# Kernel optimization log

Hardware: AMD Instinct MI355X
Metric: run time of the kernel (lower is better)

## Reference

```python
import jax, jax.numpy as jnp
import numpy as np

NX = 320   # image matrix (nRead)
NC = 8     # coils
NT = 8     # motion states
M = 65536  # non-Cartesian k-space samples per frame
OS = 2     # gridding oversampling factor


def setup_inputs() -> dict:
    key = jax.random.key(0)
    ks = jax.random.split(key, 7)
    kspace_r = jax.random.normal(ks[0], (NC, M), jnp.float32)
    kspace_i = jax.random.normal(ks[1], (NC, M), jnp.float32)
    # k-space trajectory normalized to [-0.5, 0.5)
    traj = jax.random.uniform(ks[2], (M, 2, NT), jnp.float32, -0.5, 0.5)
    csm_r = jax.random.normal(ks[3], (NC, NX, NX), jnp.float32)
    csm_i = jax.random.normal(ks[4], (NC, NX, NX), jnp.float32)
    dcf = jax.random.uniform(ks[5], (M, NT), jnp.float32)
    # motion/flow field in pixels, [NX, NX, 2, NT]
    motions = 3.0 * jax.random.normal(ks[6], (NX, NX, 2, NT), jnp.float32)
    return dict(kspace_r=kspace_r, kspace_i=kspace_i, traj=traj,
                csm_r=csm_r, csm_i=csm_i, dcf=dcf, motions=motions)


def _grid_adjoint(kspace, traj_t, dcf_t, csm):
    """Adjoint NUFFT (gpuNUFFT adj_op): density-compensated bilinear gridding
    onto a 2x oversampled Cartesian grid, inverse FFT, center crop,
    deapodization, and conjugate coil combination."""
    G = OS * NX
    data = (kspace * dcf_t[None, :]).astype(jnp.complex64)  # [NC, M]
    u = (traj_t[:, 0] + 0.5) * G
    v = (traj_t[:, 1] + 0.5) * G
    u0 = jnp.floor(u)
    v0 = jnp.floor(v)
    du = (u - u0).astype(jnp.float32)
    dv = (v - v0).astype(jnp.float32)
    i0 = u0.astype(jnp.int32) % G
    i1 = (i0 + 1) % G
    j0 = v0.astype(jnp.int32) % G
    j1 = (j0 + 1) % G
    grid = jnp.zeros((NC, G, G), jnp.complex64)
    grid = grid.at[:, i0, j0].add(data * ((1.0 - du) * (1.0 - dv)))
    grid = grid.at[:, i1, j0].add(data * (du * (1.0 - dv)))
    grid = grid.at[:, i0, j1].add(data * ((1.0 - du) * dv))
    grid = grid.at[:, i1, j1].add(data * (du * dv))
    im_os = jnp.fft.fftshift(
        jnp.fft.ifft2(jnp.fft.ifftshift(grid, axes=(-2, -1)), axes=(-2, -1)),
        axes=(-2, -1))
    s = (G - NX) // 2
    im = im_os[:, s:s + NX, s:s + NX]  # [NC, NX, NX]
    # deapodization: FT of the triangle (bilinear) gridding kernel is sinc^2
    x = (jnp.arange(NX, dtype=jnp.float32) - NX // 2) / G
    d = jnp.sinc(x) ** 2
    im = im / (d[:, None] * d[None, :])
    # conjugate coil combine with sensitivity maps
    return jnp.sum(jnp.conj(csm) * im, axis=0).astype(jnp.complex64)


def _bilinear_warp(im, flow):
    """apply_sparse_motion: sparse bilinear-interpolation warp of a 2D image
    by a per-pixel displacement field flow[..., 0:2] (in pixels)."""
    Nx, Ny = im.shape
    xs = jnp.arange(Nx, dtype=jnp.float32)[:, None] + flow[..., 0]
    ys = jnp.arange(Ny, dtype=jnp.float32)[None, :] + flow[..., 1]
    xs = jnp.clip(xs, 0.0, Nx - 1.0)
    ys = jnp.clip(ys, 0.0, Ny - 1.0)
    x0 = jnp.floor(xs).astype(jnp.int32)
    y0 = jnp.floor(ys).astype(jnp.int32)
    x1 = jnp.minimum(x0 + 1, Nx - 1)
    y1 = jnp.minimum(y0 + 1, Ny - 1)
    dx = xs - x0.astype(jnp.float32)
    dy = ys - y0.astype(jnp.float32)
    return ((1.0 - dx) * (1.0 - dy) * im[x0, y0]
            + dx * (1.0 - dy) * im[x1, y0]
            + (1.0 - dx) * dy * im[x0, y1]
            + dx * dy * im[x1, y1])


def reference(kspace_r, kspace_i, traj, csm_r, csm_i, dcf, motions):
    kspace = (kspace_r + 1j * kspace_i).astype(jnp.complex64)
    csm = (csm_r + 1j * csm_i).astype(jnp.complex64)

    def frame(traj_t, dcf_t, flow_t):
        im = _grid_adjoint(kspace, traj_t, dcf_t, csm)
        return _bilinear_warp(im, flow_t)

    # vmap over motion states: traj[..., t], dcf[..., t], motions[..., t]
    per_frame = jax.vmap(frame, in_axes=(2, 1, 3))(traj, dcf, motions)  # [NT, NX, NX]
    out = jnp.sum(per_frame, axis=0)  # temporal sum, complex [NX, NX]
    return jnp.stack([out.real, out.imag], axis=-1)  # [NX, NX, 2]
```

## Files before the change

kernel.cpp:

```cpp
#include <hip/hip_runtime.h>
#include <math.h>

#define NXI 320
#define NCI 8
#define NTI 8
#define MI  65536
#define GI  640
#define G2I (GI*GI)
#define NPIX (NXI*NXI)
#define REC_F 20
#define NBINS (NTI*G2I)
#define SCAN_BLKS2 (NBINS/4096)

typedef float v2f __attribute__((ext_vector_type(2)));

__device__ inline v2f cmul(v2f a, v2f b) {
    v2f axx = __builtin_shufflevector(a, a, 0, 0);
    v2f ayy = __builtin_shufflevector(a, a, 1, 1);
    v2f byx = __builtin_shufflevector(b, b, 1, 0);
    v2f r = axx * b;
    v2f t = ayy * byx;
    return r + v2f{-t.x, t.y};
}

template<int H>
__device__ inline float sxf(float x) {
    if constexpr (H == 1) {
        return __int_as_float(__builtin_amdgcn_update_dpp(
            __float_as_int(x), __float_as_int(x), 0xB1, 0xF, 0xF, false));
    } else if constexpr (H == 2) {
        return __int_as_float(__builtin_amdgcn_update_dpp(
            __float_as_int(x), __float_as_int(x), 0x4E, 0xF, 0xF, false));
    } else if constexpr (H == 8) {
        return __int_as_float(__builtin_amdgcn_update_dpp(
            __float_as_int(x), __float_as_int(x), 0x128, 0xF, 0xF, false));
    } else {
        return __shfl_xor(x, H, 64);
    }
}
template<int H>
__device__ inline v2f sxv(v2f v) { return v2f{sxf<H>(v.x), sxf<H>(v.y)}; }

__device__ inline void cell_of(const float* __restrict__ traj, int m, int f,
                               int& i0s, int& j0s, float& du, float& dv)
{
    float tu = traj[(m*2 + 0)*NTI + f];
    float tv = traj[(m*2 + 1)*NTI + f];
    float u = (tu + 0.5f) * (float)GI;
    float v = (tv + 0.5f) * (float)GI;
    float fu = floorf(u), fv = floorf(v);
    du = u - fu; dv = v - fv;
    i0s = (int)fu + GI/2; if (i0s >= GI) i0s -= GI;
    j0s = (int)fv + GI/2; if (j0s >= GI) j0s -= GI;
}

__global__ __launch_bounds__(256) void count_cells(
    const float* __restrict__ traj, int* __restrict__ counts)
{
    int tid = blockIdx.x * 256 + threadIdx.x;
    int f = tid >> 16, m = tid & (MI - 1);
    int i0s, j0s; float du, dv;
    cell_of(traj, m, f, i0s, j0s, du, dv);
    atomicAdd(&counts[f*G2I + i0s*GI + j0s], 1);
}

__device__ inline int wave_incl_scan(int v, int lane) {
    #pragma unroll
    for (int d = 1; d < 64; d <<= 1) {
        int y = __shfl_up(v, d, 64);
        if (lane >= d) v += y;
    }
    return v;
}

__global__ __launch_bounds__(1024) void scanA(const int4* __restrict__ counts4,
                                              int4* __restrict__ binstart4,
                                              int* __restrict__ sums)
{
    __shared__ int wtot[16];
    int tid = threadIdx.x, lane = tid & 63, wv = tid >> 6;
    int i = blockIdx.x * 1024 + tid;
    int4 c = counts4[i];
    int s = c.x + c.y + c.z + c.w;
    int incl = wave_incl_scan(s, lane);
    if (lane == 63) wtot[wv] = incl;
    __syncthreads();
    if (wv == 0 && lane < 16) {
        int t = wtot[lane];
        #pragma unroll
        for (int d = 1; d < 16; d <<= 1) {
            int y = __shfl_up(t, d, 64);
            if (lane >= d) t += y;
        }
        wtot[lane] = t;
    }
    __syncthreads();
    int woff = wv ? wtot[wv - 1] : 0;
    int excl = woff + incl - s;
    int4 b;
    b.x = excl; b.y = excl + c.x; b.z = b.y + c.y; b.w = b.z + c.z;
    binstart4[i] = b;
    if (tid == 1023) sums[blockIdx.x] = woff + incl;
}

__global__ __launch_bounds__(1024) void scanB(int* __restrict__ sums,
                                              int* __restrict__ binstart)
{
    __shared__ int tmp[1024];
    int tid = threadIdx.x;
    int v = (tid < SCAN_BLKS2) ? sums[tid] : 0;
    tmp[tid] = v; __syncthreads();
    for (int d = 1; d < 1024; d <<= 1) {
        int y = (tid >= d) ? tmp[tid - d] : 0;
        __syncthreads();
        tmp[tid] += y;
        __syncthreads();
    }
    int incl = tmp[tid];
    if (tid < SCAN_BLKS2) sums[tid] = incl - v;
    if (tid == SCAN_BLKS2 - 1) {
        sums[SCAN_BLKS2] = incl;
        binstart[NBINS] = 0;
    }
}

__global__ __launch_bounds__(256) void scatter_cells(
    const float* __restrict__ kr, const float* __restrict__ ki,
    const float* __restrict__ traj, const float* __restrict__ dcf,
    int* __restrict__ counts, const int* __restrict__ binstart,
    const int* __restrict__ sums, float* __restrict__ recs)
{
    int tid = blockIdx.x * 256 + threadIdx.x;
    int f = tid >> 16, m = tid & (MI - 1);
    int i0s, j0s; float du, dv;
    cell_of(traj, m, f, i0s, j0s, du, dv);
    float w = dcf[m*NTI + f];
    int bin = f*G2I + i0s*GI + j0s;
    int within = atomicSub(&counts[bin], 1) - 1;
    int slot = binstart[bin] + sums[bin >> 12] + within;
    float4* r = (float4*)(recs + (size_t)slot * REC_F);
    r[0] = make_float4(du, 1.f - du, dv, 1.f - dv);
    #pragma unroll
    for (int q = 0; q < 4; ++q) {
        int c0 = 2*q;
        r[1+q] = make_float4(kr[c0*MI + m]*w,     ki[c0*MI + m]*w,
                             kr[(c0+1)*MI + m]*w, ki[(c0+1)*MI + m]*w);
    }
}

__device__ inline void dft5p(v2f x0, v2f x1, v2f x2, v2f x3, v2f x4, v2f* X)
{
    const float c1 = 0.309016994f, c2 = -0.809016994f;
    const float s1 = 0.951056516f, s2 =  0.587785252f;
    v2f S1 = x1 + x4, D1 = x1 - x4;
    v2f S2 = x2 + x3, D2 = x2 - x3;
    X[0] = x0 + S1 + S2;
    v2f A = x0 + c1*S1 + c2*S2;
    v2f T = s1*D1 + s2*D2;
    v2f B = x0 + c2*S1 + c1*S2;
    v2f U = s2*D1 - s1*D2;
    v2f iT = v2f{-T.y, T.x};
    v2f iU = v2f{-U.y, U.x};
    X[1] = A + iT;  X[4] = A - iT;
    X[2] = B + iU;  X[3] = B - iU;
}

template<int H, int S>
__device__ inline void bf_stage(v2f* a, int lane)
{
    const float PI = 3.14159265358979f;
    bool low = (lane & H) == 0;
    int kp = (lane << S) & 31;
    float sn, cs;
    __sincosf((2.0f * PI / 64.0f) * (float)kp, &sn, &cs);
    v2f w = low ? v2f{1.f, 0.f} : v2f{cs, sn};
    float sg = low ? 1.f : -1.f;
    v2f sgv = v2f{sg, sg};
    #pragma unroll
    for (int n = 0; n < 10; ++n) {
        v2f p = sxv<H>(a[n]);
        v2f t = sgv * a[n] + p;
        a[n] = cmul(t, w);
    }
}

__device__ inline void fft640_pruned(v2f* a, int lane, v2f* line, int xorm)
{
    const float PI = 3.14159265358979f;
    bf_stage<32, 0>(a, lane);
    bf_stage<16, 1>(a, lane);
    bf_stage< 8, 2>(a, lane);
    bf_stage< 4, 3>(a, lane);
    bf_stage< 2, 4>(a, lane);
    bf_stage< 1, 5>(a, lane);
    int k1 = __brev(lane) >> 26;
    float th2 = (2.0f * PI / 640.0f) * (float)k1;
    float sn, cs;
    __sincosf(th2, &sn, &cs);
    v2f wb = v2f{cs, sn};
    v2f w = wb;
    #pragma unroll
    for (int n = 1; n < 10; ++n) {
        a[n] = cmul(a[n], w);
        w = cmul(w, wb);
    }
    v2f E[5], O[5];
    dft5p(a[0], a[2], a[4], a[6], a[8], E);
    dft5p(a[1], a[3], a[5], a[7], a[9], O);
    const v2f tk1 = { 0.809016994f, 0.587785252f};
    const v2f tk2 = { 0.309016994f, 0.951056516f};
    const v2f tk3 = {-0.309016994f, 0.951056516f};
    const v2f tk4 = {-0.809016994f, 0.587785252f};
    v2f t1 = cmul(tk1, O[1]);
    v2f t2 = cmul(tk2, O[2]);
    v2f t3 = cmul(tk3, O[3]);
    v2f t4 = cmul(tk4, O[4]);
    bool hi = (k1 >= 32);
    line[(160 + k1) ^ xorm] = E[0] + O[0];
    line[(224 + k1) ^ xorm] = E[1] + t1;
    int yx = hi ? (k1 - 32) : (288 + k1);
    v2f zx = hi ? (E[2] - t2) : (E[2] + t2);
    line[yx ^ xorm] = zx;
    line[(32 + k1) ^ xorm] = E[3] - t3;
    line[(96 + k1) ^ xorm] = E[4] - t4;
}

__global__ __launch_bounds__(512, 8) void row_fft(
    const int* __restrict__ binstart, const int* __restrict__ sums,
    const float* __restrict__ recs, v2f* __restrict__ rowout)
{
    __shared__ v2f A[NCI][GI];
    int bid = blockIdx.x;
    int i = bid % GI;
    int f = bid / GI;
    int tid = threadIdx.x;
    int im1 = i ? i - 1 : GI - 1;
    const int base0 = f*G2I + i*GI;
    const int base1 = f*G2I + im1*GI;

    #define GS(b) (binstart[b] + sums[(b) >> 12])

    for (int j = tid; j < GI; j += 512) {
        v2f acc[NCI];
        #pragma unroll
        for (int c = 0; c < NCI; ++c) acc[c] = v2f{0.f, 0.f};
        if (j > 0) {
            int lo0 = GS(base0 + j - 1), mid0 = GS(base0 + j), hi0 = GS(base0 + j + 1);
            int lo1 = GS(base1 + j - 1), mid1 = GS(base1 + j), hi1 = GS(base1 + j + 1);
            int L0 = hi0 - lo0;
            int K  = L0 + (hi1 - lo1);
            for (int k = 0; k < K; ++k) {
                bool p1 = (k >= L0);
                int  s   = p1 ? (lo1 + (k - L0)) : (lo0 + k);
                int  mid = p1 ? mid1 : mid0;
                const float4* R = (const float4*)(recs + (size_t)s*REC_F);
                float4 h4 = R[0];
                float wr = p1 ? h4.x : h4.y;
                float w  = wr * ((s < mid) ? h4.z : h4.w);
                float4 d0 = R[1], d1 = R[2], d2 = R[3], d3 = R[4];
                acc[0] += w * v2f{d0.x, d0.y};  acc[1] += w * v2f{d0.z, d0.w};
                acc[2] += w * v2f{d1.x, d1.y};  acc[3] += w * v2f{d1.z, d1.w};
                acc[4] += w * v2f{d2.x, d2.y};  acc[5] += w * v2f{d2.z, d2.w};
                acc[6] += w * v2f{d3.x, d3.y};  acc[7] += w * v2f{d3.z, d3.w};
            }
        } else {
            #pragma unroll
            for (int p = 0; p < 2; ++p) {
                const int base = p ? base1 : base0;
                #pragma unroll
                for (int side = 0; side < 2; ++side) {
                    int b = base + (side ? 0 : (GI - 1));
                    int s0 = GS(b), s1 = GS(b + 1);
                    for (int s = s0; s < s1; ++s) {
                        const float4* R = (const float4*)(recs + (size_t)s*REC_F);
                        float4 h4 = R[0];
                        float wr = p ? h4.x : h4.y;
                        float w  = wr * (side ? h4.w : h4.z);
                        float4 d0 = R[1], d1 = R[2], d2 = R[3], d3 = R[4];
                        acc[0] += w * v2f{d0.x, d0.y};  acc[1] += w * v2f{d0.z, d0.w};
                        acc[2] += w * v2f{d1.x, d1.y};  acc[3] += w * v2f{d1.z, d1.w};
                        acc[4] += w * v2f{d2.x, d2.y};  acc[5] += w * v2f{d2.z, d2.w};
                        acc[6] += w * v2f{d3.x, d3.y};  acc[7] += w * v2f{d3.z, d3.w};
                    }
                }
            }
        }
        #pragma unroll
        for (int c = 0; c < NCI; ++c) A[c][j] = acc[c];
    }
    #undef GS
    __syncthreads();

    int wv = tid >> 6, lane = tid & 63;
    v2f a[10];
    #pragma unroll
    for (int n = 0; n < 10; ++n) a[n] = A[wv][10*lane + n];
    fft640_pruned(a, lane, A[wv], 0);
    v2f* dst = rowout + (((size_t)f*NCI + wv)*GI + i)*NXI;
    #pragma unroll
    for (int q = 0; q < 5; ++q) {
        int yc = lane + 64*q;
        dst[yc] = A[wv][yc];
    }
}

__global__ __launch_bounds__(512, 8) void col_fft(
    const v2f* __restrict__ rowout, v2f* __restrict__ colimg)
{
    __shared__ v2f A[8][GI];
    int bid = blockIdx.x;
    int g = bid % 40;
    int c = (bid / 40) % NCI;
    int f = bid / (40*NCI);
    int y0 = g * 8;
    int tid = threadIdx.x;
    const v2f* src = rowout + ((size_t)f*NCI + c)*GI*NXI + y0;
    for (int idx = tid; idx < 8*GI; idx += 512) {
        int l = idx & 7, k = idx >> 3;
        A[l][k ^ (4*(l & 3))] = src[(size_t)k*NXI + l];
    }
    __syncthreads();
    int wv = tid >> 6, lane = tid & 63;
    int xm = 4 * (wv & 3);
    v2f a[10];
    #pragma unroll
    for (int n = 0; n < 10; ++n) a[n] = A[wv][(10*lane + n) ^ xm];
    fft640_pruned(a, lane, A[wv], xm);
    __syncthreads();
    v2f* dst = colimg + ((size_t)f*NCI + c)*NPIX + y0;
    for (int idx = tid; idx < 8*NXI; idx += 512) {
        int l = idx & 7, xx = idx >> 3;
        dst[(size_t)xx*NXI + l] = A[l][xx ^ (4*(l & 3))];
    }
}

__global__ __launch_bounds__(256) void combine_kernel(
    const float2* __restrict__ colimg, const float* __restrict__ csr,
    const float* __restrict__ csi, float2* __restrict__ img)
{
    int f = blockIdx.y;
    int pix = blockIdx.x * 256 + threadIdx.x;
    int x = pix / NXI, y = pix - x*NXI;
    const float PI = 3.14159265358979f;
    float tx = (x - 160) * (1.0f/GI);
    float ty = (y - 160) * (1.0f/GI);
    float dx = 1.0f, dy = 1.0f;
    if (x != 160) { float s = __sinf(PI*tx) / (PI*tx); dx = s*s; }
    if (y != 160) { float s = __sinf(PI*ty) / (PI*ty); dy = s*s; }
    float scale = 1.0f / ((float)G2I * dx * dy);
    float accr = 0.f, acci = 0.f;
    #pragma unroll
    for (int c = 0; c < NCI; ++c) {
        float2 g = colimg[((size_t)f*NCI + c)*NPIX + pix];
        float cr = csr[c*NPIX + pix];
        float ci = csi[c*NPIX + pix];
        accr += cr*g.x + ci*g.y;
        acci += cr*g.y - ci*g.x;
    }
    img[(size_t)f*NPIX + pix] = make_float2(accr*scale, acci*scale);
}

__global__ __launch_bounds__(256) void warp_sum(
    const float2* __restrict__ img, const float* __restrict__ motions,
    float* __restrict__ out)
{
    int pix = blockIdx.x * 256 + threadIdx.x;
    int x = pix / NXI, y = pix - x*NXI;
    float accr = 0.f, acci = 0.f;
    #pragma unroll
    for (int f = 0; f < NTI; ++f) {
        float fx = motions[(size_t)(pix*2 + 0)*NTI + f];
        float fy = motions[(size_t)(pix*2 + 1)*NTI + f];
        float xs = fminf(fmaxf((float)x + fx, 0.0f), (float)(NXI-1));
        float ys = fminf(fmaxf((float)y + fy, 0.0f), (float)(NXI-1));
        int x0 = (int)floorf(xs);
        int y0 = (int)floorf(ys);
        int x1 = min(x0+1, NXI-1);
        int y1 = min(y0+1, NXI-1);
        float dx = xs - (float)x0;
        float dy = ys - (float)y0;
        const float2* im = img + (size_t)f*NPIX;
        float2 v00 = im[x0*NXI + y0];
        float2 v10 = im[x1*NXI + y0];
        float2 v01 = im[x0*NXI + y1];
        float2 v11 = im[x1*NXI + y1];
        float w00 = (1.f-dx)*(1.f-dy), w10 = dx*(1.f-dy);
        float w01 = (1.f-dx)*dy,       w11 = dx*dy;
        accr += w00*v00.x + w10*v10.x + w01*v01.x + w11*v11.x;
        acci += w00*v00.y + w10*v10.y + w01*v01.y + w11*v11.y;
    }
    out[pix*2+0] = accr;
    out[pix*2+1] = acci;
}

extern "C" void kernel_launch(void* const* d_in, const int* in_sizes, int n_in,
                              void* d_out, int out_size, void* d_ws, size_t ws_size,
                              hipStream_t stream)
{
    const float* kr   = (const float*)d_in[0];
    const float* ki   = (const float*)d_in[1];
    const float* traj = (const float*)d_in[2];
    const float* csr  = (const float*)d_in[3];
    const float* csi  = (const float*)d_in[4];
    const float* dcf  = (const float*)d_in[5];
    const float* mot  = (const float*)d_in[6];
    float* out = (float*)d_out;

    char* ws = (char*)d_ws;
    float*  recs     = (float*)ws;
    ws += (size_t)NTI * MI * REC_F * sizeof(float);
    v2f*    rowout   = (v2f*)ws;
    ws += (size_t)NTI * NCI * GI * NXI * sizeof(float2);
    float2* colimg   = (float2*)ws;
    ws += (size_t)NTI * NCI * NPIX * sizeof(float2);
    float2* img      = (float2*)ws;
    ws += (size_t)NTI * NPIX * sizeof(float2);
    int*    counts   = (int*)ws;  ws += (size_t)NBINS * sizeof(int);
    int*    binstart = (int*)ws;  ws += ((size_t)NBINS + 16) * sizeof(int);
    int*    sums     = (int*)ws;  ws += 16384;

    hipMemsetAsync(counts, 0, (size_t)NBINS * sizeof(int), stream);
    count_cells  <<<NTI*MI/256, 256, 0, stream>>>(traj, counts);
    scanA        <<<SCAN_BLKS2, 1024, 0, stream>>>((const int4*)counts,
                                                   (int4*)binstart, sums);
    scanB        <<<1,          1024, 0, stream>>>(sums, binstart);
    scatter_cells<<<NTI*MI/256, 256, 0, stream>>>(kr, ki, traj, dcf, counts,
                                                  binstart, sums, recs);
    row_fft      <<<NTI*GI,     512, 0, stream>>>(binstart, sums, recs, rowout);
    col_fft      <<<NTI*NCI*40, 512, 0, stream>>>(rowout, (v2f*)colimg);
    combine_kernel<<<dim3(NPIX/256, NTI), 256, 0, stream>>>(colimg, csr, csi, img);
    warp_sum     <<<NPIX/256,   256, 0, stream>>>(img, mot, out);
}
```

Before: 280.7 us.

## Fuse column FFT with coil combine and move deapodization into warp

The column FFT kernel now loops over four coils per block and accumulates the conjugate coil-sensitivity combination in registers, writing two partial images (one per coil half) instead of a full per-coil image. The separate combine kernel and the large per-coil intermediate buffer are removed. Deapodization scaling moves into the warp kernel as a separable per-row/column table folded into the interpolation weights, and that kernel now gathers from both partial images. This cuts a global round trip of the per-coil image, but launches far fewer col-FFT blocks (640 instead of 2560) with serialized coil loops and extra barriers, and doubles the gathers in the warp.

```diff
diff --git a/kernel.cpp b/kernel.cpp
--- a/kernel.cpp
+++ b/kernel.cpp
@@ -304,67 +304,74 @@
     }
 }
 
-__global__ __launch_bounds__(512, 8) void col_fft(
-    const v2f* __restrict__ rowout, v2f* __restrict__ colimg)
+__global__ __launch_bounds__(512, 8) void col_fft_combine(
+    const v2f* __restrict__ rowout, const float* __restrict__ csr,
+    const float* __restrict__ csi, float2* __restrict__ img2)
 {
     __shared__ v2f A[8][GI];
     int bid = blockIdx.x;
     int g = bid % 40;
-    int c = (bid / 40) % NCI;
-    int f = bid / (40*NCI);
+    int h = (bid / 40) & 1;
+    int f = bid / 80;
     int y0 = g * 8;
+    int c0 = h * 4;
     int tid = threadIdx.x;
-    const v2f* src = rowout + ((size_t)f*NCI + c)*GI*NXI + y0;
-    for (int idx = tid; idx < 8*GI; idx += 512) {
-        int l = idx & 7, k = idx >> 3;
-        A[l][k ^ (4*(l & 3))] = src[(size_t)k*NXI + l];
-    }
-    __syncthreads();
     int wv = tid >> 6, lane = tid & 63;
     int xm = 4 * (wv & 3);
-    v2f a[10];
-    #pragma unroll
-    for (int n = 0; n < 10; ++n) a[n] = A[wv][(10*lane + n) ^ xm];
-    fft640_pruned(a, lane, A[wv], xm);
+
+    v2f acc[5];
+    #pragma unroll
+    for (int q = 0; q < 5; ++q) acc[q] = v2f{0.f, 0.f};
+
+    for (int cc = 0; cc < 4; ++cc) {
+        int c = c0 + cc;
+        const v2f* src = rowout + ((size_t)f*NCI + c)*GI*NXI + y0;
+        for (int idx = tid; idx < 8*GI; idx += 512) {
+            int l = idx & 7, k = idx >> 3;
+            A[l][k ^ (4*(l & 3))] = src[(size_t)k*NXI + l];
+        }
+        __syncthreads();
+        v2f a[10];
+        #pragma unroll
+        for (int n = 0; n < 10; ++n) a[n] = A[wv][(10*lane + n) ^ xm];
+        fft640_pruned(a, lane, A[wv], xm);
+        __syncthreads();
+        const float* cr = csr + (size_t)c*NPIX;
+        const float* ci = csi + (size_t)c*NPIX;
+        #pragma unroll
+        for (int q = 0; q < 5; ++q) {
+            int P = tid + 512*q; int x = P >> 3, l = P & 7;
+            v2f gv = A[l][x ^ (4*(l & 3))];
+            int pix = x*NXI + y0 + l;
+            float crv = cr[pix], civ = ci[pix];
+            acc[q].x += crv*gv.x + civ*gv.y;
+            acc[q].y += crv*gv.y - civ*gv.x;
+        }
+        __syncthreads();
+    }
+    float2* dst = img2 + ((size_t)h*NTI + f) * NPIX;
+    #pragma unroll
+    for (int q = 0; q < 5; ++q) {
+        int P = tid + 512*q; int x = P >> 3, l = P & 7;
+        dst[(size_t)x*NXI + y0 + l] = make_float2(acc[q].x, acc[q].y);
+    }
+}
+
+__global__ __launch_bounds__(256) void warp_sum(
+    const float2* __restrict__ img2, const float* __restrict__ motions,
+    float* __restrict__ out)
+{
+    __shared__ float sdinv[NXI];
+    int tid = threadIdx.x;
+    const float PI = 3.14159265358979f;
+    for (int idx = tid; idx < NXI; idx += 256) {
+        float t = (idx - 160) * (1.0f/GI);
+        float d = 1.0f;
+        if (idx != 160) { float s = __sinf(PI*t) / (PI*t); d = s*s; }
+        sdinv[idx] = (1.0f/GI) / d;
+    }
     __syncthreads();
-    v2f* dst = colimg + ((size_t)f*NCI + c)*NPIX + y0;
-    for (int idx = tid; idx < 8*NXI; idx += 512) {
-        int l = idx & 7, xx = idx >> 3;
-        dst[(size_t)xx*NXI + l] = A[l][xx ^ (4*(l & 3))];
-    }
-}
-
-__global__ __launch_bounds__(256) void combine_kernel(
-    const float2* __restrict__ colimg, const float* __restrict__ csr,
-    const float* __restrict__ csi, float2* __restrict__ img)
-{
-    int f = blockIdx.y;
-    int pix = blockIdx.x * 256 + threadIdx.x;
-    int x = pix / NXI, y = pix - x*NXI;
-    const float PI = 3.14159265358979f;
-    float tx = (x - 160) * (1.0f/GI);
-    float ty = (y - 160) * (1.0f/GI);
-    float dx = 1.0f, dy = 1.0f;
-    if (x != 160) { float s = __sinf(PI*tx) / (PI*tx); dx = s*s; }
-    if (y != 160) { float s = __sinf(PI*ty) / (PI*ty); dy = s*s; }
-    float scale = 1.0f / ((float)G2I * dx * dy);
-    float accr = 0.f, acci = 0.f;
-    #pragma unroll
-    for (int c = 0; c < NCI; ++c) {
-        float2 g = colimg[((size_t)f*NCI + c)*NPIX + pix];
-        float cr = csr[c*NPIX + pix];
-        float ci = csi[c*NPIX + pix];
-        accr += cr*g.x + ci*g.y;
-        acci += cr*g.y - ci*g.x;
-    }
-    img[(size_t)f*NPIX + pix] = make_float2(accr*scale, acci*scale);
-}
-
-__global__ __launch_bounds__(256) void warp_sum(
-    const float2* __restrict__ img, const float* __restrict__ motions,
-    float* __restrict__ out)
-{
-    int pix = blockIdx.x * 256 + threadIdx.x;
+    int pix = blockIdx.x * 256 + tid;
     int x = pix / NXI, y = pix - x*NXI;
     float accr = 0.f, acci = 0.f;
     #pragma unroll
@@ -379,15 +386,20 @@
         int y1 = min(y0+1, NXI-1);
         float dx = xs - (float)x0;
         float dy = ys - (float)y0;
-        const float2* im = img + (size_t)f*NPIX;
-        float2 v00 = im[x0*NXI + y0];
-        float2 v10 = im[x1*NXI + y0];
-        float2 v01 = im[x0*NXI + y1];
-        float2 v11 = im[x1*NXI + y1];
-        float w00 = (1.f-dx)*(1.f-dy), w10 = dx*(1.f-dy);
-        float w01 = (1.f-dx)*dy,       w11 = dx*dy;
-        accr += w00*v00.x + w10*v10.x + w01*v01.x + w11*v11.x;
-        acci += w00*v00.y + w10*v10.y + w01*v01.y + w11*v11.y;
+        float ax0 = sdinv[x0], ax1 = sdinv[x1];
+        float ay0 = sdinv[y0], ay1 = sdinv[y1];
+        float w00 = (1.f-dx)*(1.f-dy)*ax0*ay0, w10 = dx*(1.f-dy)*ax1*ay0;
+        float w01 = (1.f-dx)*dy*ax0*ay1,       w11 = dx*dy*ax1*ay1;
+        #pragma unroll
+        for (int h = 0; h < 2; ++h) {
+            const float2* im = img2 + ((size_t)h*NTI + f)*NPIX;
+            float2 v00 = im[x0*NXI + y0];
+            float2 v10 = im[x1*NXI + y0];
+            float2 v01 = im[x0*NXI + y1];
+            float2 v11 = im[x1*NXI + y1];
+            accr += w00*v00.x + w10*v10.x + w01*v01.x + w11*v11.x;
+            acci += w00*v00.y + w10*v10.y + w01*v01.y + w11*v11.y;
+        }
     }
     out[pix*2+0] = accr;
     out[pix*2+1] = acci;
@@ -411,10 +423,8 @@
     ws += (size_t)NTI * MI * REC_F * sizeof(float);
     v2f*    rowout   = (v2f*)ws;
     ws += (size_t)NTI * NCI * GI * NXI * sizeof(float2);
-    float2* colimg   = (float2*)ws;
-    ws += (size_t)NTI * NCI * NPIX * sizeof(float2);
-    float2* img      = (float2*)ws;
-    ws += (size_t)NTI * NPIX * sizeof(float2);
+    float2* img2     = (float2*)ws;
+    ws += (size_t)2 * NTI * NPIX * sizeof(float2);
     int*    counts   = (int*)ws;  ws += (size_t)NBINS * sizeof(int);
     int*    binstart = (int*)ws;  ws += ((size_t)NBINS + 16) * sizeof(int);
     int*    sums     = (int*)ws;  ws += 16384;
@@ -427,7 +437,6 @@
     scatter_cells<<<NTI*MI/256, 256, 0, stream>>>(kr, ki, traj, dcf, counts,
                                                   binstart, sums, recs);
     row_fft      <<<NTI*GI,     512, 0, stream>>>(binstart, sums, recs, rowout);
-    col_fft      <<<NTI*NCI*40, 512, 0, stream>>>(rowout, (v2f*)colimg);
-    combine_kernel<<<dim3(NPIX/256, NTI), 256, 0, stream>>>(colimg, csr, csi, img);
-    warp_sum     <<<NPIX/256,   256, 0, stream>>>(img, mot, out);
-}
+    col_fft_combine<<<NTI*2*40, 512, 0, stream>>>(rowout, csr, csi, img2);
+    warp_sum     <<<NPIX/256,   256, 0, stream>>>(img2, mot, out);
+}
```

New measurement: 352.5 us. 1.26x slower.
